# Kernel tuning notes

Measured on AMD Instinct MI355X. Metric: run time of the kernel, lower is better.

The kernel has to match this reference:

```python
import jax, jax.numpy as jnp
import numpy as np

N_HEADS = 16
NEG_INF = jnp.float32(-1e9)


def split_heads(x, h):
    # (b, t, h*d) -> (b*h, t, d)
    b, t, e = x.shape
    return x.reshape(b, t, h, e // h).transpose(0, 2, 1, 3).reshape(b * h, t, e // h)


def setup_inputs() -> dict:
    key = jax.random.key(0)
    ks = jax.random.split(key, 8)
    B, T, E = 1, 2048, 1024
    QK, V, NB, ML = 1024, 1024, 10, 2048
    g = lambda k, shp, sc: jax.random.normal(k, shp, jnp.float32) * sc
    return {
        "X_bte": g(ks[0], (B, T, E), 1.0),
        "W_q": g(ks[1], (E, QK), 0.02),
        "b_q": jnp.zeros((QK,), jnp.float32),
        "W_k": g(ks[2], (E, QK), 0.02),
        "W_v": g(ks[3], (E, V), 0.02),
        "W_proj": g(ks[4], (V, E), 0.02),
        "b_proj": jnp.zeros((E,), jnp.float32),
        "W_r": g(ks[5], (E, NB * N_HEADS), 0.02),
        "b_r": jnp.zeros((NB * N_HEADS,), jnp.float32),
        "b_nd": g(ks[6], (NB, ML), 0.2),  # B_SCALE = 0.2
    }


def relattn_logits(X_bte, W_r, b_r, b_nd):
    # R_btn: per-head mixing coefficients over the n_basis banded bias rows
    R_btn = split_heads(X_bte @ W_r + b_r, N_HEADS)      # (B*h, t, n_basis)
    t = R_btn.shape[1]
    T = t  # self-attention, no cache
    max_len = b_nd.shape[1]
    # Fused form of einsum('btn,ntT->btT', R, bandify(b_nd,t,T)):
    # first contract bases, then gather the Toeplitz diagonal d = i - j.
    P_btd = jnp.einsum('btn,nd->btd', R_btn, b_nd)       # (B*h, t, max_len)
    i = jnp.arange(t)[:, None]
    j = jnp.arange(T)[None, :]
    rel = i - j                                          # time difference
    valid = (rel >= 0) & (rel < max_len)
    idx = jnp.clip(rel, 0, max_len - 1)
    extra_btT = jnp.where(valid, P_btd[:, i, idx], jnp.float32(0.0))
    return extra_btT                                     # (B*h, t, T)


def reference(X_bte, W_q, b_q, W_k, W_v, W_proj, b_proj, W_r, b_r, b_nd):
    B, t, _ = X_bte.shape
    Q = split_heads(X_bte @ W_q + b_q, N_HEADS)          # (B*h, t, dqk)
    K = split_heads(X_bte @ W_k, N_HEADS)                # k_layer has no bias
    Vh = split_heads(X_bte @ W_v, N_HEADS)               # v_layer has no bias
    d = Q.shape[-1]

    extra_btT = relattn_logits(X_bte, W_r, b_r, b_nd)
    logits = jnp.einsum('bqd,bkd->bqk', Q, K) / jnp.sqrt(jnp.float32(d)) + extra_btT
    causal = jnp.tril(jnp.ones((t, t), bool))
    logits = jnp.where(causal, logits, NEG_INF)
    A = jax.nn.softmax(logits, axis=-1)                  # (B*h, t, t)
    out = jnp.einsum('bqk,bkd->bqd', A, Vh)              # (B*h, t, dv)
    out = out.reshape(B, N_HEADS, t, -1).transpose(0, 2, 1, 3).reshape(B, t, -1)
    return out @ W_proj + b_proj                          # (B, t, x_size)
```

## Files before the change

### kernel.cpp

```cpp
#include <hip/hip_runtime.h>
#include <hip/hip_bf16.h>
#include <math.h>


typedef __attribute__((ext_vector_type(8))) short bf16x8;
typedef __attribute__((ext_vector_type(4))) float f32x4;

#define MFMA16(a,b,c) __builtin_amdgcn_mfma_f32_16x16x32_bf16((a),(b),(c),0,0,0)
#define GLB(p)  ((const __attribute__((address_space(1))) void*)(p))
#define LDSP(p) ((__attribute__((address_space(3))) void*)(p))
#define LDY2 3328

__device__ __forceinline__ unsigned short f2bf(float x){
  unsigned u = __float_as_uint(x);
  u = (u + 0x7FFFu + ((u >> 16) & 1u)) >> 16;
  return (unsigned short)u;
}
__device__ __forceinline__ unsigned short f2bf_rn(float x){
  __hip_bfloat16 b = __float2bfloat16(x);
  return *reinterpret_cast<unsigned short*>(&b);
}
__device__ __forceinline__ float bf2f(unsigned short b){
  return __uint_as_float(((unsigned)b) << 16);
}


__global__ __launch_bounds__(256) void prep_mega(
    const float* __restrict__ X,
    const float* __restrict__ Wq, const float* __restrict__ Wk,
    const float* __restrict__ Wv, const float* __restrict__ Wr,
    const float* __restrict__ Wp,
    const float* __restrict__ bq, const float* __restrict__ br,
    unsigned short* __restrict__ Xb, unsigned short* __restrict__ WbT,
    unsigned short* __restrict__ WpT, float* __restrict__ bias)
{
  __shared__ float tile[64][65];
  const int b = blockIdx.x;
  const int tid = threadIdx.x;

  if (b < 1024){
    const int i = (b * 256 + tid) * 8;
    f32x4 a = *(const f32x4*)(X + i);
    f32x4 v2 = *(const f32x4*)(X + i + 4);
    bf16x8 v;
    v[0]=(short)f2bf(a.x); v[1]=(short)f2bf(a.y); v[2]=(short)f2bf(a.z); v[3]=(short)f2bf(a.w);
    v[4]=(short)f2bf(v2.x); v[5]=(short)f2bf(v2.y); v[6]=(short)f2bf(v2.z); v[7]=(short)f2bf(v2.w);
    *(bf16x8*)(Xb + i) = v;
    return;
  }
  if (b < 1024 + 832){
    const int idx = b - 1024;
    const int k0 = (idx & 15) * 64, c0 = (idx >> 4) * 64;
    {
      const int r = tid >> 2, cs = (tid & 3) << 4;
      #pragma unroll
      for (int q = 0; q < 4; ++q){
        const int c = c0 + cs + q * 4;
        f32x4 v;
        if (c < 1024){
          v = *(const f32x4*)(Wq + (size_t)(k0+r)*1024 + c);
          v.x *= 0.125f; v.y *= 0.125f; v.z *= 0.125f; v.w *= 0.125f;
        }
        else if (c < 2048) v = *(const f32x4*)(Wk + (size_t)(k0+r)*1024 + (c-1024));
        else if (c < 3072) v = *(const f32x4*)(Wv + (size_t)(k0+r)*1024 + (c-2048));
        else if (c < 3232) v = *(const f32x4*)(Wr + (size_t)(k0+r)*160  + (c-3072));
        else               v = (f32x4){0.f,0.f,0.f,0.f};
        tile[r][cs+q*4+0]=v.x; tile[r][cs+q*4+1]=v.y; tile[r][cs+q*4+2]=v.z; tile[r][cs+q*4+3]=v.w;
      }
    }
    __syncthreads();
    const int c = tid >> 2, ks = (tid & 3) << 4;
    bf16x8 o0, o1;
    #pragma unroll
    for (int x = 0; x < 8; ++x) o0[x] = (short)f2bf(tile[ks + x][c]);
    #pragma unroll
    for (int x = 0; x < 8; ++x) o1[x] = (short)f2bf(tile[ks + 8 + x][c]);
    *(bf16x8*)(WbT + (size_t)(c0 + c) * 1024 + k0 + ks)     = o0;
    *(bf16x8*)(WbT + (size_t)(c0 + c) * 1024 + k0 + ks + 8) = o1;
    return;
  }
  if (b < 1024 + 832 + 256){
    const int idx = b - 1856;
    const int k0 = (idx & 15) * 64, c0 = (idx >> 4) * 64;
    {
      const int r = tid >> 2, cs = (tid & 3) << 4;
      #pragma unroll
      for (int q = 0; q < 4; ++q){
        f32x4 v = *(const f32x4*)(Wp + (size_t)(k0+r)*1024 + c0 + cs + q*4);
        tile[r][cs+q*4+0]=v.x; tile[r][cs+q*4+1]=v.y; tile[r][cs+q*4+2]=v.z; tile[r][cs+q*4+3]=v.w;
      }
    }
    __syncthreads();
    const int c = tid >> 2, ks = (tid & 3) << 4;
    bf16x8 o0, o1;
    #pragma unroll
    for (int x = 0; x < 8; ++x) o0[x] = (short)f2bf(tile[ks + x][c]);
    #pragma unroll
    for (int x = 0; x < 8; ++x) o1[x] = (short)f2bf(tile[ks + 8 + x][c]);
    *(bf16x8*)(WpT + (size_t)(c0 + c) * 1024 + k0 + ks)     = o0;
    *(bf16x8*)(WpT + (size_t)(c0 + c) * 1024 + k0 + ks + 8) = o1;
    return;
  }
  const int c = (b - 2112) * 256 + tid;
  if (c < 3328){
    float v = 0.f;
    if (c < 1024) v = bq[c] * 0.125f;
    else if (c >= 3072 && c < 3232) v = br[c - 3072];
    bias[c] = v;
  }
}


__global__ __launch_bounds__(256) void post_mega(
    const unsigned short* __restrict__ Y, const float* __restrict__ bnd,
    unsigned short* __restrict__ Vt, unsigned short* __restrict__ BndT)
{
  __shared__ unsigned short tile[64][72];
  const int b = blockIdx.x;
  const int tid = threadIdx.x;

  if (b < 512){
    const int h = b >> 5, t0 = (b & 31) * 64;
    {
      const int r = tid >> 2, cs = (tid & 3) << 4;
      const unsigned short* src = Y + (size_t)(t0 + r) * LDY2 + 2048 + h * 64 + cs;
      *(bf16x8*)&tile[r][cs]     = *(const bf16x8*)src;
      *(bf16x8*)&tile[r][cs + 8] = *(const bf16x8*)(src + 8);
    }
    __syncthreads();
    const int d = tid >> 2, ts = (tid & 3) << 4;
    bf16x8 o0, o1;
    #pragma unroll
    for (int x = 0; x < 8; ++x) o0[x] = (short)tile[ts + x][d];
    #pragma unroll
    for (int x = 0; x < 8; ++x) o1[x] = (short)tile[ts + 8 + x][d];
    *(bf16x8*)(Vt + (size_t)(h*64 + d) * 2048 + t0 + ts)     = o0;
    *(bf16x8*)(Vt + (size_t)(h*64 + d) * 2048 + t0 + ts + 8) = o1;
    return;
  }
  const int t = (b - 512) * 256 + tid;
  if (t >= 2176) return;
  const int rel = t - 64;
  unsigned short* dst = BndT + (size_t)t * 32;
  bf16x8 v0 = {}, v1 = {}, z = {};
  if (rel >= 0 && rel < 2048){
    #pragma unroll
    for (int n = 0; n < 8; ++n) v0[n] = (short)f2bf(bnd[n * 2048 + rel]);
    v1[0] = (short)f2bf(bnd[8 * 2048 + rel]);
    v1[1] = (short)f2bf(bnd[9 * 2048 + rel]);
  }
  *(bf16x8*)dst        = v0;
  *(bf16x8*)(dst + 8)  = v1;
  *(bf16x8*)(dst + 16) = z;
  *(bf16x8*)(dst + 24) = z;
}


__global__ __launch_bounds__(256) void gemm_bf16(
    const unsigned short* __restrict__ A,
    const unsigned short* __restrict__ BT,
    const float* __restrict__ bias,
    unsigned short* __restrict__ C, int ldc)
{
  __shared__ unsigned short As[128 * 64];
  __shared__ unsigned short Bs[128 * 64];
  const int tid = threadIdx.x;
  const int w = tid >> 6, lane = tid & 63;
  const int lid = lane & 15, lgrp = lane >> 4;
  const int wm = w >> 1, wn = w & 1;
  const int row0 = blockIdx.y << 7, col0 = blockIdx.x << 7;
  const int sr = lane >> 3;
  const int sc = (lane & 7) ^ sr;

  f32x4 acc[4][4] = {};

  for (int k0 = 0; k0 < 1024; k0 += 64){
    #pragma unroll
    for (int it = 0; it < 4; ++it){
      const int r0w = (w << 5) + (it << 3);
      const int r = r0w + sr;
      __builtin_amdgcn_global_load_lds(GLB(A  + (size_t)(row0 + r) * 1024 + k0 + (sc << 3)),
                                       LDSP(&As[r0w << 6]), 16, 0, 0);
      __builtin_amdgcn_global_load_lds(GLB(BT + (size_t)(col0 + r) * 1024 + k0 + (sc << 3)),
                                       LDSP(&Bs[r0w << 6]), 16, 0, 0);
    }
    __syncthreads();

    bf16x8 af[4][2], bfr[4][2];
    #pragma unroll
    for (int m = 0; m < 4; ++m){
      const int ra = wm * 64 + m * 16 + lid;
      const int rb = wn * 64 + m * 16 + lid;
      #pragma unroll
      for (int kk = 0; kk < 2; ++kk){
        const int kc = kk * 4 + lgrp;
        af[m][kk]  = *(const bf16x8*)&As[(ra << 6) + ((kc ^ (lid & 7)) << 3)];
        bfr[m][kk] = *(const bf16x8*)&Bs[(rb << 6) + ((kc ^ (lid & 7)) << 3)];
      }
    }
    #pragma unroll
    for (int m = 0; m < 4; ++m)
      #pragma unroll
      for (int n = 0; n < 4; ++n){
        acc[m][n] = MFMA16(af[m][0], bfr[n][0], acc[m][n]);
        acc[m][n] = MFMA16(af[m][1], bfr[n][1], acc[m][n]);
      }
    __syncthreads();
  }

  #pragma unroll
  for (int m = 0; m < 4; ++m){
    #pragma unroll
    for (int n = 0; n < 4; ++n){
      const int col = col0 + wn * 64 + n * 16 + lid;
      const float bv = bias[col];
      #pragma unroll
      for (int i = 0; i < 4; ++i){
        const int row = row0 + wm * 64 + m * 16 + lgrp * 4 + i;
        C[(size_t)row * ldc + col] = f2bf(acc[m][n][i] + bv);
      }
    }
  }
}


__global__ __launch_bounds__(256) void gemm_bf16_out(
    const unsigned short* __restrict__ A,
    const unsigned short* __restrict__ BT,
    const float* __restrict__ bias,
    float* __restrict__ C)
{
  __shared__ unsigned short As[64 * 64];
  __shared__ unsigned short Bs[128 * 64];
  const int tid = threadIdx.x;
  const int w = tid >> 6, lane = tid & 63;
  const int lid = lane & 15, lgrp = lane >> 4;
  const int wm = w >> 1, wn = w & 1;
  const int row0 = blockIdx.y << 6, col0 = blockIdx.x << 7;
  const int sr = lane >> 3;
  const int sc = (lane & 7) ^ sr;

  f32x4 acc[2][4] = {};

  for (int k0 = 0; k0 < 1024; k0 += 64){
    #pragma unroll
    for (int it = 0; it < 2; ++it){
      const int r0w = (w << 4) + (it << 3);
      const int r = r0w + sr;
      __builtin_amdgcn_global_load_lds(GLB(A + (size_t)(row0 + r) * 1024 + k0 + (sc << 3)),
                                       LDSP(&As[r0w << 6]), 16, 0, 0);
    }
    #pragma unroll
    for (int it = 0; it < 4; ++it){
      const int r0w = (w << 5) + (it << 3);
      const int r = r0w + sr;
      __builtin_amdgcn_global_load_lds(GLB(BT + (size_t)(col0 + r) * 1024 + k0 + (sc << 3)),
                                       LDSP(&Bs[r0w << 6]), 16, 0, 0);
    }
    __syncthreads();

    bf16x8 af[2][2], bfr[4][2];
    #pragma unroll
    for (int m = 0; m < 2; ++m){
      const int ra = wm * 32 + m * 16 + lid;
      #pragma unroll
      for (int kk = 0; kk < 2; ++kk){
        const int kc = kk * 4 + lgrp;
        af[m][kk] = *(const bf16x8*)&As[(ra << 6) + ((kc ^ (lid & 7)) << 3)];
      }
    }
    #pragma unroll
    for (int n = 0; n < 4; ++n){
      const int rb = wn * 64 + n * 16 + lid;
      #pragma unroll
      for (int kk = 0; kk < 2; ++kk){
        const int kc = kk * 4 + lgrp;
        bfr[n][kk] = *(const bf16x8*)&Bs[(rb << 6) + ((kc ^ (lid & 7)) << 3)];
      }
    }
    #pragma unroll
    for (int m = 0; m < 2; ++m)
      #pragma unroll
      for (int n = 0; n < 4; ++n){
        acc[m][n] = MFMA16(af[m][0], bfr[n][0], acc[m][n]);
        acc[m][n] = MFMA16(af[m][1], bfr[n][1], acc[m][n]);
      }
    __syncthreads();
  }

  #pragma unroll
  for (int m = 0; m < 2; ++m){
    #pragma unroll
    for (int n = 0; n < 4; ++n){
      const int col = col0 + wn * 64 + n * 16 + lid;
      const float bv = bias[col];
      #pragma unroll
      for (int i = 0; i < 4; ++i){
        const int row = row0 + wm * 32 + m * 16 + lgrp * 4 + i;
        C[(size_t)row * 1024 + col] = acc[m][n][i] + bv;
      }
    }
  }
}


__global__ __launch_bounds__(256) void attn_mfma(
    const unsigned short* __restrict__ Y,
    const unsigned short* __restrict__ Vt,
    const unsigned short* __restrict__ BndT,
    unsigned short* __restrict__ AO)
{
  __shared__ unsigned short KV[4][4096];
  __shared__ unsigned short UN[4][1280];

  const int id = blockIdx.x;
  const int h = id & 15;
  const int u = id >> 4;
  const int p = u >> 1, qh = u & 1;
  const int tid = threadIdx.x;
  const int w = tid >> 6, lane = tid & 63;
  const int wq = w & 1, grp = w >> 1;
  const int lid = lane & 15, lgrp = lane >> 4;
  const int sr = lane >> 3;
  const int scc = (lane & 7) ^ sr;

  unsigned short* Ksg = &KV[grp][0];
  unsigned short* Vsg = &KV[2 + grp][0];
  unsigned short* un  = &UN[w][0];

  #pragma unroll
  for (int seg = 0; seg < 2; ++seg){
    const int qb = seg ? (31 - p) : p;
    const int q0b = qb * 64 + qh * 32;
    const int nt = qb + 1;
    const int L = (nt + 1) >> 1;

    const int qrow = q0b + wq * 16 + lid;
    bf16x8 qf[2];
    #pragma unroll
    for (int kk = 0; kk < 2; ++kk)
      qf[kk] = *(const bf16x8*)(Y + (size_t)qrow * LDY2 + h*64 + ((kk*4 + lgrp) << 3));

    bf16x8 rf = {};
    {
      const unsigned* rp = (const unsigned*)(Y + (size_t)qrow * LDY2 + 3072 + h*10);
      if (lgrp == 0){
        #pragma unroll
        for (int x = 0; x < 4; ++x) ((unsigned*)&rf)[x] = rp[x];
      } else if (lgrp == 1){
        ((unsigned*)&rf)[0] = rp[4];
      }
    }

    float m_i = -INFINITY, l_i = 0.f;
    f32x4 o[4] = {};

    for (int it = 0; it < L; ++it){
      const int kb = 2 * it + grp;
      const bool active = (kb < nt);
      const int j0 = kb << 6;
      const int d0 = q0b - j0;

      if (active){
        #pragma unroll
        for (int st = 0; st < 4; ++st){
          const int r0w = wq * 32 + st * 8;
          const int r = r0w + sr;
          __builtin_amdgcn_global_load_lds(GLB(Y  + (size_t)(j0 + r) * LDY2 + 1024 + h*64 + (scc << 3)),
                                           LDSP(&Ksg[r0w << 6]), 16, 0, 0);
          __builtin_amdgcn_global_load_lds(GLB(Vt + (size_t)(h*64 + r) * 2048 + j0 + (scc << 3)),
                                           LDSP(&Vsg[r0w << 6]), 16, 0, 0);
        }
      }
      __syncthreads();

      if (active){
        bf16x8 bw[5];
        #pragma unroll
        for (int f = 0; f < 5; ++f){
          const int rowt = d0 + 1 + (wq + f) * 16 + lid;
          bw[f] = *(const bf16x8*)(BndT + ((size_t)rowt << 5) + (lgrp << 3));
        }

        f32x4 s[4] = {};
        __builtin_amdgcn_s_setprio(1);
        #pragma unroll
        for (int kk = 0; kk < 2; ++kk){
          const int kc = kk * 4 + lgrp;
          #pragma unroll
          for (int n4 = 0; n4 < 4; ++n4){
            const bf16x8 kf = *(const bf16x8*)&Ksg[((n4*16 + lid) << 6) + ((kc ^ (lid & 7)) << 3)];
            s[n4] = MFMA16(kf, qf[kk], s[n4]);
          }
        }
        __builtin_amdgcn_s_setprio(0);

        #pragma unroll
        for (int f = 0; f < 5; ++f){
          f32x4 ef = {};
          ef = MFMA16(rf, bw[f], ef);
          #pragma unroll
          for (int i = 0; i < 4; ++i)
            un[(lgrp*4 + i) * 80 + f*16 + lid] = f2bf_rn(ef[i]);
        }

        const bool diag = (kb == qb);
        const int ql = qh*32 + wq*16 + lid;
        #pragma unroll
        for (int n4 = 0; n4 < 4; ++n4){
          #pragma unroll
          for (int i = 0; i < 4; ++i){
            const int jl = n4*16 + lgrp*4 + i;
            float v = s[n4][i] + bf2f(un[lid * 80 + (lid - jl + 63)]);
            if (diag && jl > ql) v = -1e9f;
            s[n4][i] = v;
          }
        }

        float rm = s[0][0];
        #pragma unroll
        for (int n4 = 0; n4 < 4; ++n4)
          #pragma unroll
          for (int i = 0; i < 4; ++i) rm = fmaxf(rm, s[n4][i]);
        rm = fmaxf(rm, __shfl_xor(rm, 16));
        rm = fmaxf(rm, __shfl_xor(rm, 32));

        if (__all(rm - m_i <= 8.f)){
          float rs = 0.f;
          #pragma unroll
          for (int n4 = 0; n4 < 4; ++n4)
            #pragma unroll
            for (int i = 0; i < 4; ++i){
              const float pv = __expf(s[n4][i] - m_i);
              s[n4][i] = pv;
              rs += pv;
            }
          rs += __shfl_xor(rs, 16);
          rs += __shfl_xor(rs, 32);
          l_i += rs;
        } else {
          const float mn = fmaxf(m_i, rm);
          const float sc_ = __expf(m_i - mn);
          m_i = mn;
          float rs = 0.f;
          #pragma unroll
          for (int n4 = 0; n4 < 4; ++n4)
            #pragma unroll
            for (int i = 0; i < 4; ++i){
              const float pv = __expf(s[n4][i] - mn);
              s[n4][i] = pv;
              rs += pv;
            }
          rs += __shfl_xor(rs, 16);
          rs += __shfl_xor(rs, 32);
          l_i = l_i * sc_ + rs;
          #pragma unroll
          for (int n4 = 0; n4 < 4; ++n4)
            #pragma unroll
            for (int i = 0; i < 4; ++i) o[n4][i] *= sc_;
        }

        #pragma unroll
        for (int n4 = 0; n4 < 4; ++n4){
          const unsigned a = ((unsigned)f2bf_rn(s[n4][0])) | (((unsigned)f2bf_rn(s[n4][1])) << 16);
          const unsigned b = ((unsigned)f2bf_rn(s[n4][2])) | (((unsigned)f2bf_rn(s[n4][3])) << 16);
          const int chunk = (n4*2 + (lgrp >> 1)) ^ (lid & 7);
          const int base = (lid << 6) + (chunk << 3) + ((lgrp & 1) << 2);
          *(unsigned*)&un[base]     = a;
          *(unsigned*)&un[base + 2] = b;
        }

        __builtin_amdgcn_s_setprio(1);
        #pragma unroll
        for (int kk = 0; kk < 2; ++kk){
          const int kc = kk * 4 + lgrp;
          const bf16x8 pb = *(const bf16x8*)&un[(lid << 6) + ((kc ^ (lid & 7)) << 3)];
          #pragma unroll
          for (int n4 = 0; n4 < 4; ++n4){
            const bf16x8 vf = *(const bf16x8*)&Vsg[((n4*16 + lid) << 6) + ((kc ^ (lid & 7)) << 3)];
            o[n4] = MFMA16(vf, pb, o[n4]);
          }
        }
        __builtin_amdgcn_s_setprio(0);
      }
      __syncthreads();
    }

    float* oScr  = (float*)&KV[0][0];
    float* mlScr = oScr + 2 * 16 * 68;
    if (grp == 1){
      const int base = (wq * 16 + lid) * 68;
      #pragma unroll
      for (int n4 = 0; n4 < 4; ++n4)
        *(f32x4*)&oScr[base + n4*16 + lgrp*4] = o[n4];
      if (lgrp == 0){
        mlScr[(wq * 16 + lid) * 2 + 0] = m_i;
        mlScr[(wq * 16 + lid) * 2 + 1] = l_i;
      }
    }
    __syncthreads();
    if (grp == 0){
      const int base = (wq * 16 + lid) * 68;
      const float m1 = mlScr[(wq * 16 + lid) * 2 + 0];
      const float l1 = mlScr[(wq * 16 + lid) * 2 + 1];
      const float M  = fmaxf(m_i, m1);
      const float a  = __expf(m_i - M);
      const float b  = __expf(m1 - M);
      const float inv = 1.f / (l_i * a + l1 * b);
      unsigned short* dst = AO + (size_t)qrow * 1024 + h * 64;
      #pragma unroll
      for (int n4 = 0; n4 < 4; ++n4){
        const f32x4 o1 = *(const f32x4*)&oScr[base + n4*16 + lgrp*4];
        const float v0 = (o[n4][0]*a + o1[0]*b) * inv;
        const float v1 = (o[n4][1]*a + o1[1]*b) * inv;
        const float v2 = (o[n4][2]*a + o1[2]*b) * inv;
        const float v3 = (o[n4][3]*a + o1[3]*b) * inv;
        unsigned r0 = ((unsigned)f2bf_rn(v0)) | (((unsigned)f2bf_rn(v1)) << 16);
        unsigned r1 = ((unsigned)f2bf_rn(v2)) | (((unsigned)f2bf_rn(v3)) << 16);
        unsigned long long pk = ((unsigned long long)r1 << 32) | r0;
        *(unsigned long long*)(dst + n4*16 + lgrp*4) = pk;
      }
    }
    __syncthreads();
  }
}


extern "C" void kernel_launch(void* const* d_in, const int* in_sizes, int n_in,
                              void* d_out, int out_size, void* d_ws, size_t ws_size,
                              hipStream_t stream) {
  const float* X   = (const float*)d_in[0];
  const float* Wq  = (const float*)d_in[1];
  const float* bq  = (const float*)d_in[2];
  const float* Wk  = (const float*)d_in[3];
  const float* Wv  = (const float*)d_in[4];
  const float* Wp  = (const float*)d_in[5];
  const float* bp  = (const float*)d_in[6];
  const float* Wr  = (const float*)d_in[7];
  const float* br  = (const float*)d_in[8];
  const float* bnd = (const float*)d_in[9];
  float* out = (float*)d_out;

  unsigned short* Xb  = (unsigned short*)d_ws;
  unsigned short* WbT = Xb  + (size_t)2048 * 1024;
  unsigned short* Yb  = WbT + (size_t)3328 * 1024;
  unsigned short* Vt  = Yb  + (size_t)2048 * 3328;
  unsigned short* WpT = Vt  + (size_t)1024 * 2048;
  float* bias = (float*)(WpT + (size_t)1024 * 1024);
  unsigned short* AO   = Xb;
  unsigned short* BndT = WbT + (size_t)3232 * 1024;

  prep_mega    <<<2125,         256, 0, stream>>>(X, Wq, Wk, Wv, Wr, Wp, bq, br,
                                                  Xb, WbT, WpT, bias);
  gemm_bf16    <<<dim3(26, 16), 256, 0, stream>>>(Xb, WbT, bias, Yb, 3328);
  post_mega    <<<521,          256, 0, stream>>>(Yb, bnd, Vt, BndT);
  attn_mfma    <<<512,          256, 0, stream>>>(Yb, Vt, BndT, AO);
  gemm_bf16_out<<<dim3(8, 32),  256, 0, stream>>>(AO, WpT, bp, out);
}
```

Before: 111.7 us.

## Restructure attention into single-wave blocks, one 16-row query tile each

Replaces the 256-thread attention blocks, which split the key range across two wave groups, paired a short and a long query block for load balance, and merged results in LDS, with 64-thread single-wave blocks. Each block owns 16 query rows of one head and walks all causal key tiles sequentially, loading K/V into private LDS and waiting on vmcnt instead of using __syncthreads. The grid is ordered longest query blocks first so the heavy work is scheduled early. This removes block-level barriers and the cross-group merge, but loses the intra-block key split and reloads each K/V tile in four separate blocks, raising global and L2 traffic and serialising load latency within each wave.

```diff
diff --git a/kernel.cpp b/kernel.cpp
--- a/kernel.cpp
+++ b/kernel.cpp
@@ -304,224 +304,198 @@
 }
 
 
-__global__ __launch_bounds__(256) void attn_mfma(
+__device__ __forceinline__ void attn_tile_body(
+    const unsigned short* __restrict__ Ksb,
+    const unsigned short* __restrict__ Vsb,
+    unsigned short* __restrict__ un,
+    const bf16x8 (&bw)[5],
+    const bf16x8 (&qf)[2], const bf16x8& rf,
+    int lid, int lgrp,
+    bool diag, int ql,
+    float& m_i, float& l_i, f32x4 (&o)[4])
+{
+  f32x4 s[4] = {};
+  __builtin_amdgcn_s_setprio(1);
+  #pragma unroll
+  for (int kk = 0; kk < 2; ++kk){
+    const int kc = kk * 4 + lgrp;
+    #pragma unroll
+    for (int n4 = 0; n4 < 4; ++n4){
+      const bf16x8 kf = *(const bf16x8*)&Ksb[((n4*16 + lid) << 6) + ((kc ^ (lid & 7)) << 3)];
+      s[n4] = MFMA16(kf, qf[kk], s[n4]);
+    }
+  }
+  __builtin_amdgcn_s_setprio(0);
+
+  #pragma unroll
+  for (int f = 0; f < 5; ++f){
+    f32x4 ef = {};
+    ef = MFMA16(rf, bw[f], ef);
+    #pragma unroll
+    for (int i = 0; i < 4; ++i)
+      un[(lgrp*4 + i) * 80 + f*16 + lid] = f2bf_rn(ef[i]);
+  }
+
+  #pragma unroll
+  for (int n4 = 0; n4 < 4; ++n4){
+    #pragma unroll
+    for (int i = 0; i < 4; ++i){
+      const int jl = n4*16 + lgrp*4 + i;
+      float v = s[n4][i] + bf2f(un[lid * 80 + (lid - jl + 63)]);
+      if (diag && jl > ql) v = -1e9f;
+      s[n4][i] = v;
+    }
+  }
+
+  float rm = s[0][0];
+  #pragma unroll
+  for (int n4 = 0; n4 < 4; ++n4)
+    #pragma unroll
+    for (int i = 0; i < 4; ++i) rm = fmaxf(rm, s[n4][i]);
+  rm = fmaxf(rm, __shfl_xor(rm, 16));
+  rm = fmaxf(rm, __shfl_xor(rm, 32));
+
+  if (__all(rm - m_i <= 8.f)){
+    float rs = 0.f;
+    #pragma unroll
+    for (int n4 = 0; n4 < 4; ++n4)
+      #pragma unroll
+      for (int i = 0; i < 4; ++i){
+        const float pv = __expf(s[n4][i] - m_i);
+        s[n4][i] = pv;
+        rs += pv;
+      }
+    rs += __shfl_xor(rs, 16);
+    rs += __shfl_xor(rs, 32);
+    l_i += rs;
+  } else {
+    const float mn = fmaxf(m_i, rm);
+    const float sc_ = __expf(m_i - mn);
+    m_i = mn;
+    float rs = 0.f;
+    #pragma unroll
+    for (int n4 = 0; n4 < 4; ++n4)
+      #pragma unroll
+      for (int i = 0; i < 4; ++i){
+        const float pv = __expf(s[n4][i] - mn);
+        s[n4][i] = pv;
+        rs += pv;
+      }
+    rs += __shfl_xor(rs, 16);
+    rs += __shfl_xor(rs, 32);
+    l_i = l_i * sc_ + rs;
+    #pragma unroll
+    for (int n4 = 0; n4 < 4; ++n4)
+      #pragma unroll
+      for (int i = 0; i < 4; ++i) o[n4][i] *= sc_;
+  }
+
+  #pragma unroll
+  for (int n4 = 0; n4 < 4; ++n4){
+    const unsigned a = ((unsigned)f2bf_rn(s[n4][0])) | (((unsigned)f2bf_rn(s[n4][1])) << 16);
+    const unsigned b = ((unsigned)f2bf_rn(s[n4][2])) | (((unsigned)f2bf_rn(s[n4][3])) << 16);
+    const int chunk = (n4*2 + (lgrp >> 1)) ^ (lid & 7);
+    const int base = (lid << 6) + (chunk << 3) + ((lgrp & 1) << 2);
+    *(unsigned*)&un[base]     = a;
+    *(unsigned*)&un[base + 2] = b;
+  }
+
+  __builtin_amdgcn_s_setprio(1);
+  #pragma unroll
+  for (int kk = 0; kk < 2; ++kk){
+    const int kc = kk * 4 + lgrp;
+    const bf16x8 pb = *(const bf16x8*)&un[(lid << 6) + ((kc ^ (lid & 7)) << 3)];
+    #pragma unroll
+    for (int n4 = 0; n4 < 4; ++n4){
+      const bf16x8 vf = *(const bf16x8*)&Vsb[((n4*16 + lid) << 6) + ((kc ^ (lid & 7)) << 3)];
+      o[n4] = MFMA16(vf, pb, o[n4]);
+    }
+  }
+  __builtin_amdgcn_s_setprio(0);
+}
+
+__global__ __launch_bounds__(64) void attn_mfma(
     const unsigned short* __restrict__ Y,
     const unsigned short* __restrict__ Vt,
     const unsigned short* __restrict__ BndT,
     unsigned short* __restrict__ AO)
 {
-  __shared__ unsigned short KV[4][4096];
-  __shared__ unsigned short UN[4][1280];
+  __shared__ unsigned short Ks[64 * 64];
+  __shared__ unsigned short Vs[64 * 64];
+  __shared__ unsigned short UN[1280];
 
   const int id = blockIdx.x;
-  const int h = id & 15;
-  const int u = id >> 4;
-  const int p = u >> 1, qh = u & 1;
-  const int tid = threadIdx.x;
-  const int w = tid >> 6, lane = tid & 63;
-  const int wq = w & 1, grp = w >> 1;
+  const int qb = 31 - (id >> 6);
+  const int rest = id & 63;
+  const int u = rest >> 4;
+  const int h = rest & 15;
+  const int lane = threadIdx.x;
   const int lid = lane & 15, lgrp = lane >> 4;
   const int sr = lane >> 3;
   const int scc = (lane & 7) ^ sr;
 
-  unsigned short* Ksg = &KV[grp][0];
-  unsigned short* Vsg = &KV[2 + grp][0];
-  unsigned short* un  = &UN[w][0];
-
-  #pragma unroll
-  for (int seg = 0; seg < 2; ++seg){
-    const int qb = seg ? (31 - p) : p;
-    const int q0b = qb * 64 + qh * 32;
-    const int nt = qb + 1;
-    const int L = (nt + 1) >> 1;
-
-    const int qrow = q0b + wq * 16 + lid;
-    bf16x8 qf[2];
-    #pragma unroll
-    for (int kk = 0; kk < 2; ++kk)
-      qf[kk] = *(const bf16x8*)(Y + (size_t)qrow * LDY2 + h*64 + ((kk*4 + lgrp) << 3));
-
-    bf16x8 rf = {};
-    {
-      const unsigned* rp = (const unsigned*)(Y + (size_t)qrow * LDY2 + 3072 + h*10);
-      if (lgrp == 0){
-        #pragma unroll
-        for (int x = 0; x < 4; ++x) ((unsigned*)&rf)[x] = rp[x];
-      } else if (lgrp == 1){
-        ((unsigned*)&rf)[0] = rp[4];
-      }
-    }
-
-    float m_i = -INFINITY, l_i = 0.f;
-    f32x4 o[4] = {};
-
-    for (int it = 0; it < L; ++it){
-      const int kb = 2 * it + grp;
-      const bool active = (kb < nt);
-      const int j0 = kb << 6;
-      const int d0 = q0b - j0;
-
-      if (active){
-        #pragma unroll
-        for (int st = 0; st < 4; ++st){
-          const int r0w = wq * 32 + st * 8;
-          const int r = r0w + sr;
-          __builtin_amdgcn_global_load_lds(GLB(Y  + (size_t)(j0 + r) * LDY2 + 1024 + h*64 + (scc << 3)),
-                                           LDSP(&Ksg[r0w << 6]), 16, 0, 0);
-          __builtin_amdgcn_global_load_lds(GLB(Vt + (size_t)(h*64 + r) * 2048 + j0 + (scc << 3)),
-                                           LDSP(&Vsg[r0w << 6]), 16, 0, 0);
-        }
-      }
-      __syncthreads();
-
-      if (active){
-        bf16x8 bw[5];
-        #pragma unroll
-        for (int f = 0; f < 5; ++f){
-          const int rowt = d0 + 1 + (wq + f) * 16 + lid;
-          bw[f] = *(const bf16x8*)(BndT + ((size_t)rowt << 5) + (lgrp << 3));
-        }
-
-        f32x4 s[4] = {};
-        __builtin_amdgcn_s_setprio(1);
-        #pragma unroll
-        for (int kk = 0; kk < 2; ++kk){
-          const int kc = kk * 4 + lgrp;
-          #pragma unroll
-          for (int n4 = 0; n4 < 4; ++n4){
-            const bf16x8 kf = *(const bf16x8*)&Ksg[((n4*16 + lid) << 6) + ((kc ^ (lid & 7)) << 3)];
-            s[n4] = MFMA16(kf, qf[kk], s[n4]);
-          }
-        }
-        __builtin_amdgcn_s_setprio(0);
-
-        #pragma unroll
-        for (int f = 0; f < 5; ++f){
-          f32x4 ef = {};
-          ef = MFMA16(rf, bw[f], ef);
-          #pragma unroll
-          for (int i = 0; i < 4; ++i)
-            un[(lgrp*4 + i) * 80 + f*16 + lid] = f2bf_rn(ef[i]);
-        }
-
-        const bool diag = (kb == qb);
-        const int ql = qh*32 + wq*16 + lid;
-        #pragma unroll
-        for (int n4 = 0; n4 < 4; ++n4){
-          #pragma unroll
-          for (int i = 0; i < 4; ++i){
-            const int jl = n4*16 + lgrp*4 + i;
-            float v = s[n4][i] + bf2f(un[lid * 80 + (lid - jl + 63)]);
-            if (diag && jl > ql) v = -1e9f;
-            s[n4][i] = v;
-          }
-        }
-
-        float rm = s[0][0];
-        #pragma unroll
-        for (int n4 = 0; n4 < 4; ++n4)
-          #pragma unroll
-          for (int i = 0; i < 4; ++i) rm = fmaxf(rm, s[n4][i]);
-        rm = fmaxf(rm, __shfl_xor(rm, 16));
-        rm = fmaxf(rm, __shfl_xor(rm, 32));
-
-        if (__all(rm - m_i <= 8.f)){
-          float rs = 0.f;
-          #pragma unroll
-          for (int n4 = 0; n4 < 4; ++n4)
-            #pragma unroll
-            for (int i = 0; i < 4; ++i){
-              const float pv = __expf(s[n4][i] - m_i);
-              s[n4][i] = pv;
-              rs += pv;
-            }
-          rs += __shfl_xor(rs, 16);
-          rs += __shfl_xor(rs, 32);
-          l_i += rs;
-        } else {
-          const float mn = fmaxf(m_i, rm);
-          const float sc_ = __expf(m_i - mn);
-          m_i = mn;
-          float rs = 0.f;
-          #pragma unroll
-          for (int n4 = 0; n4 < 4; ++n4)
-            #pragma unroll
-            for (int i = 0; i < 4; ++i){
-              const float pv = __expf(s[n4][i] - mn);
-              s[n4][i] = pv;
-              rs += pv;
-            }
-          rs += __shfl_xor(rs, 16);
-          rs += __shfl_xor(rs, 32);
-          l_i = l_i * sc_ + rs;
-          #pragma unroll
-          for (int n4 = 0; n4 < 4; ++n4)
-            #pragma unroll
-            for (int i = 0; i < 4; ++i) o[n4][i] *= sc_;
-        }
-
-        #pragma unroll
-        for (int n4 = 0; n4 < 4; ++n4){
-          const unsigned a = ((unsigned)f2bf_rn(s[n4][0])) | (((unsigned)f2bf_rn(s[n4][1])) << 16);
-          const unsigned b = ((unsigned)f2bf_rn(s[n4][2])) | (((unsigned)f2bf_rn(s[n4][3])) << 16);
-          const int chunk = (n4*2 + (lgrp >> 1)) ^ (lid & 7);
-          const int base = (lid << 6) + (chunk << 3) + ((lgrp & 1) << 2);
-          *(unsigned*)&un[base]     = a;
-          *(unsigned*)&un[base + 2] = b;
-        }
-
-        __builtin_amdgcn_s_setprio(1);
-        #pragma unroll
-        for (int kk = 0; kk < 2; ++kk){
-          const int kc = kk * 4 + lgrp;
-          const bf16x8 pb = *(const bf16x8*)&un[(lid << 6) + ((kc ^ (lid & 7)) << 3)];
-          #pragma unroll
-          for (int n4 = 0; n4 < 4; ++n4){
-            const bf16x8 vf = *(const bf16x8*)&Vsg[((n4*16 + lid) << 6) + ((kc ^ (lid & 7)) << 3)];
-            o[n4] = MFMA16(vf, pb, o[n4]);
-          }
-        }
-        __builtin_amdgcn_s_setprio(0);
-      }
-      __syncthreads();
-    }
-
-    float* oScr  = (float*)&KV[0][0];
-    float* mlScr = oScr + 2 * 16 * 68;
-    if (grp == 1){
-      const int base = (wq * 16 + lid) * 68;
-      #pragma unroll
-      for (int n4 = 0; n4 < 4; ++n4)
-        *(f32x4*)&oScr[base + n4*16 + lgrp*4] = o[n4];
-      if (lgrp == 0){
-        mlScr[(wq * 16 + lid) * 2 + 0] = m_i;
-        mlScr[(wq * 16 + lid) * 2 + 1] = l_i;
-      }
-    }
-    __syncthreads();
-    if (grp == 0){
-      const int base = (wq * 16 + lid) * 68;
-      const float m1 = mlScr[(wq * 16 + lid) * 2 + 0];
-      const float l1 = mlScr[(wq * 16 + lid) * 2 + 1];
-      const float M  = fmaxf(m_i, m1);
-      const float a  = __expf(m_i - M);
-      const float b  = __expf(m1 - M);
-      const float inv = 1.f / (l_i * a + l1 * b);
-      unsigned short* dst = AO + (size_t)qrow * 1024 + h * 64;
-      #pragma unroll
-      for (int n4 = 0; n4 < 4; ++n4){
-        const f32x4 o1 = *(const f32x4*)&oScr[base + n4*16 + lgrp*4];
-        const float v0 = (o[n4][0]*a + o1[0]*b) * inv;
-        const float v1 = (o[n4][1]*a + o1[1]*b) * inv;
-        const float v2 = (o[n4][2]*a + o1[2]*b) * inv;
-        const float v3 = (o[n4][3]*a + o1[3]*b) * inv;
-        unsigned r0 = ((unsigned)f2bf_rn(v0)) | (((unsigned)f2bf_rn(v1)) << 16);
-        unsigned r1 = ((unsigned)f2bf_rn(v2)) | (((unsigned)f2bf_rn(v3)) << 16);
-        unsigned long long pk = ((unsigned long long)r1 << 32) | r0;
-        *(unsigned long long*)(dst + n4*16 + lgrp*4) = pk;
-      }
-    }
-    __syncthreads();
+  const int q0w = qb * 64 + u * 16;
+  const int qrow = q0w + lid;
+  const int ql = u * 16 + lid;
+  const int nt = qb + 1;
+
+  bf16x8 qf[2];
+  #pragma unroll
+  for (int kk = 0; kk < 2; ++kk)
+    qf[kk] = *(const bf16x8*)(Y + (size_t)qrow * LDY2 + h*64 + ((kk*4 + lgrp) << 3));
+
+  bf16x8 rf = {};
+  {
+    const unsigned* rp = (const unsigned*)(Y + (size_t)qrow * LDY2 + 3072 + h*10);
+    if (lgrp == 0){
+      #pragma unroll
+      for (int x = 0; x < 4; ++x) ((unsigned*)&rf)[x] = rp[x];
+    } else if (lgrp == 1){
+      ((unsigned*)&rf)[0] = rp[4];
+    }
+  }
+
+  float m_i = -INFINITY, l_i = 0.f;
+  f32x4 o[4] = {};
+
+  for (int kb = 0; kb < nt; ++kb){
+    const int j0 = kb << 6;
+    const int d0 = q0w - j0;
+
+    #pragma unroll
+    for (int st = 0; st < 8; ++st){
+      const int r0w = st * 8;
+      const int r = r0w + sr;
+      __builtin_amdgcn_global_load_lds(
+          GLB(Y + (size_t)(j0 + r) * LDY2 + 1024 + h*64 + (scc << 3)),
+          LDSP(&Ks[r0w << 6]), 16, 0, 0);
+      __builtin_amdgcn_global_load_lds(
+          GLB(Vt + (size_t)(h*64 + r) * 2048 + j0 + (scc << 3)),
+          LDSP(&Vs[r0w << 6]), 16, 0, 0);
+    }
+
+    bf16x8 bw[5];
+    #pragma unroll
+    for (int f = 0; f < 5; ++f){
+      const int rowt = d0 + 1 + f * 16 + lid;
+      bw[f] = *(const bf16x8*)(BndT + ((size_t)rowt << 5) + (lgrp << 3));
+    }
+
+    asm volatile("s_waitcnt vmcnt(0)" ::: "memory");
+    __builtin_amdgcn_sched_barrier(0);
+
+    attn_tile_body(Ks, Vs, UN, bw, qf, rf, lid, lgrp,
+                   kb == qb, ql, m_i, l_i, o);
+  }
+
+  const float inv = 1.f / l_i;
+  unsigned short* dst = AO + (size_t)qrow * 1024 + h * 64;
+  #pragma unroll
+  for (int n4 = 0; n4 < 4; ++n4){
+    unsigned r0 = ((unsigned)f2bf_rn(o[n4][0] * inv)) | (((unsigned)f2bf_rn(o[n4][1] * inv)) << 16);
+    unsigned r1 = ((unsigned)f2bf_rn(o[n4][2] * inv)) | (((unsigned)f2bf_rn(o[n4][3] * inv)) << 16);
+    unsigned long long pk = ((unsigned long long)r1 << 32) | r0;
+    *(unsigned long long*)(dst + n4*16 + lgrp*4) = pk;
   }
 }
 
@@ -554,6 +528,6 @@
                                                   Xb, WbT, WpT, bias);
   gemm_bf16    <<<dim3(26, 16), 256, 0, stream>>>(Xb, WbT, bias, Yb, 3328);
   post_mega    <<<521,          256, 0, stream>>>(Yb, bnd, Vt, BndT);
-  attn_mfma    <<<512,          256, 0, stream>>>(Yb, Vt, BndT, AO);
+  attn_mfma    <<<2048,         64,  0, stream>>>(Yb, Vt, BndT, AO);
   gemm_bf16_out<<<dim3(8, 32),  256, 0, stream>>>(AO, WpT, bp, out);
 }
```

Result: slower. 127.0 us (+13.7%).
